# Kernel tuning notes

Hardware: AMD Instinct MI355X
Metric: run time of the kernel (lower is better)

The kernel has to match this reference:

```python
import jax, jax.numpy as jnp
import numpy as np

LMBDA = 100.0
AUX_LMBDA = 25.0
REG = 1e-06
GAMMA = 0.5
EPS = 1e-10


def _safe_evals(e):
    e = jnp.nan_to_num(e, nan=EPS, posinf=1e6, neginf=EPS)
    return jnp.maximum(e, EPS)


def _mask_single(evals1, evals2):
    # evals1, evals2: [k]; returns [k, k] (rows indexed by evals2, cols by evals1)
    e1 = _safe_evals(evals1)
    e2 = _safe_evals(evals2)
    scale = jnp.maximum(jnp.maximum(e1.max(), e2.max()), 1e-10)
    g1 = (e1 / scale) ** GAMMA  # [k]
    g2 = (e2 / scale) ** GAMMA  # [k]
    d1 = g1 * g1 + 1.0
    d2 = g2 * g2 + 1.0
    M_re = (g2 / d2)[:, None] - (g1 / d1)[None, :]
    M_im = (1.0 / d2)[:, None] - (1.0 / d1)[None, :]
    M = M_re * M_re + M_im * M_im
    return jnp.nan_to_num(M, nan=0.0, posinf=1e6, neginf=0.0)


get_mask = jax.vmap(_mask_single)  # [B,k] x [B,k] -> [B,k,k]


def _solve(A, B, evals_x, evals_y, aux_evals_x, aux_evals_y):
    # A, B: [Bb, k, d]
    k = A.shape[1]
    D = LMBDA * get_mask(evals_x, evals_y)  # [Bb, k, k]
    if aux_evals_x is not None and aux_evals_y is not None:
        D = D + AUX_LMBDA * get_mask(aux_evals_x, aux_evals_y)
    AAt = jnp.einsum('bid,bjd->bij', A, A)  # [Bb, k, k]
    BAt = jnp.einsum('bid,bjd->bij', B, A)  # [Bb, k, k]
    I = jnp.eye(k, dtype=A.dtype)
    # lhs[b, i] = AAt[b] + diag(D[b, i]) + reg * I  -> [Bb, k, k, k]
    lhs = AAt[:, None, :, :] + D[:, :, :, None] * I + REG * I
    X = jnp.linalg.solve(lhs, BAt[..., None])[..., 0]  # [Bb, k, k]
    return X


def reference(feat_x, feat_y, evals_x, evals_y, evecs_x, evecs_y,
              aux_evals_x, aux_evals_y):
    A = jnp.einsum('bkn,bnd->bkd', evecs_x, feat_x)
    B = jnp.einsum('bkn,bnd->bkd', evecs_y, feat_y)
    Cxy = _solve(A, B, evals_x, evals_y, aux_evals_x, aux_evals_y)
    Cyx = _solve(B, A, evals_y, evals_x, aux_evals_y, aux_evals_x)
    return (Cxy, Cyx)


def setup_inputs() -> dict:
    key = jax.random.key(0)
    ks = jax.random.split(key, 8)
    Bb, n, d, k = 16, 4096, 512, 128
    return {
        'feat_x': jax.random.normal(ks[0], (Bb, n, d), jnp.float32),
        'feat_y': jax.random.normal(ks[1], (Bb, n, d), jnp.float32),
        'evals_x': jax.random.uniform(ks[2], (Bb, k), jnp.float32),
        'evals_y': jax.random.uniform(ks[3], (Bb, k), jnp.float32),
        'evecs_x': jax.random.normal(ks[4], (Bb, k, n), jnp.float32),
        'evecs_y': jax.random.normal(ks[5], (Bb, k, n), jnp.float32),
        'aux_evals_x': jax.random.uniform(ks[6], (Bb, k), jnp.float32),
        'aux_evals_y': jax.random.uniform(ks[7], (Bb, k), jnp.float32),
    }
```

## Files before the change

### kernel.cpp

```cpp
#include <hip/hip_runtime.h>
#include <math.h>

#define NB 16
#define NN 4096
#define DD 512
#define K128 128

__global__ __launch_bounds__(256) void gemm_proj_k(
    const float* __restrict__ feat_x, const float* __restrict__ feat_y,
    const float* __restrict__ evecs_x, const float* __restrict__ evecs_y,
    float* __restrict__ Aout, float* __restrict__ Bout)
{
    const int z = blockIdx.z;
    const int b = z & 15, which = z >> 4;
    const float* __restrict__ E = (which ? evecs_y : evecs_x) + (size_t)b * K128 * NN;
    const float* __restrict__ F = (which ? feat_y : feat_x) + (size_t)b * NN * DD;
    float* __restrict__ C = (which ? Bout : Aout) + (size_t)b * K128 * DD;
    const int i0 = blockIdx.y * 64;
    const int j0 = blockIdx.x * 128;

    __shared__ float As[32][68];
    __shared__ float Bs[32][128];

    const int t  = threadIdx.x;
    const int tm = t >> 5;
    const int tn = t & 31;

    float acc[8][4];
#pragma unroll
    for (int r = 0; r < 8; ++r)
#pragma unroll
        for (int c = 0; c < 4; ++c) acc[r][c] = 0.f;

    for (int k0 = 0; k0 < NN; k0 += 32) {
#pragma unroll
        for (int s = 0; s < 2; ++s) {
            int idx = t + s * 256;
            int i = idx >> 3, kq = idx & 7;
            float4 v = *(const float4*)(E + (size_t)(i0 + i) * NN + k0 + kq * 4);
            As[kq * 4 + 0][i] = v.x; As[kq * 4 + 1][i] = v.y;
            As[kq * 4 + 2][i] = v.z; As[kq * 4 + 3][i] = v.w;
        }
#pragma unroll
        for (int s = 0; s < 4; ++s) {
            int idx = t + s * 256;
            int kk = idx >> 5, j4 = idx & 31;
            *(float4*)&Bs[kk][j4 * 4] =
                *(const float4*)(F + (size_t)(k0 + kk) * DD + j0 + j4 * 4);
        }
        __syncthreads();
#pragma unroll
        for (int kk = 0; kk < 32; ++kk) {
            float4 a0 = *(const float4*)&As[kk][tm * 8];
            float4 a1 = *(const float4*)&As[kk][tm * 8 + 4];
            float4 b0 = *(const float4*)&Bs[kk][tn * 4];
            float av[8] = {a0.x, a0.y, a0.z, a0.w, a1.x, a1.y, a1.z, a1.w};
            float bv[4] = {b0.x, b0.y, b0.z, b0.w};
#pragma unroll
            for (int r = 0; r < 8; ++r)
#pragma unroll
                for (int c = 0; c < 4; ++c)
                    acc[r][c] = fmaf(av[r], bv[c], acc[r][c]);
        }
        __syncthreads();
    }
#pragma unroll
    for (int r = 0; r < 8; ++r) {
        float4 v = make_float4(acc[r][0], acc[r][1], acc[r][2], acc[r][3]);
        *(float4*)(C + (size_t)(i0 + tm * 8 + r) * DD + j0 + tn * 4) = v;
    }
}

__global__ __launch_bounds__(256) void gram_k(
    const float* __restrict__ A, const float* __restrict__ B,
    float* __restrict__ AAt, float* __restrict__ BBt,
    float* __restrict__ BAt, float* __restrict__ ABt)
{
    const int z = blockIdx.z;
    const int b = z & 15, g = z >> 4;
    const float* X; const float* Y; float* O;
    if (g == 0)      { X = A; Y = A; O = AAt; }
    else if (g == 1) { X = B; Y = B; O = BBt; }
    else if (g == 2) { X = B; Y = A; O = BAt; }
    else             { X = A; Y = B; O = ABt; }
    X += (size_t)b * K128 * DD; Y += (size_t)b * K128 * DD; O += (size_t)b * K128 * K128;
    const int i0 = blockIdx.y * 64, j0 = blockIdx.x * 64;

    __shared__ float Xs[32][68];
    __shared__ float Ys[32][68];

    const int t  = threadIdx.x;
    const int tm = t >> 4, tn = t & 15;

    float acc[4][4];
#pragma unroll
    for (int r = 0; r < 4; ++r)
#pragma unroll
        for (int c = 0; c < 4; ++c) acc[r][c] = 0.f;

    for (int d0 = 0; d0 < DD; d0 += 32) {
#pragma unroll
        for (int s = 0; s < 2; ++s) {
            int idx = t + s * 256;
            int i = idx >> 3, kq = idx & 7;
            float4 v = *(const float4*)(X + (size_t)(i0 + i) * DD + d0 + kq * 4);
            Xs[kq * 4 + 0][i] = v.x; Xs[kq * 4 + 1][i] = v.y;
            Xs[kq * 4 + 2][i] = v.z; Xs[kq * 4 + 3][i] = v.w;
            float4 w = *(const float4*)(Y + (size_t)(j0 + i) * DD + d0 + kq * 4);
            Ys[kq * 4 + 0][i] = w.x; Ys[kq * 4 + 1][i] = w.y;
            Ys[kq * 4 + 2][i] = w.z; Ys[kq * 4 + 3][i] = w.w;
        }
        __syncthreads();
#pragma unroll
        for (int kk = 0; kk < 32; ++kk) {
            float4 a = *(const float4*)&Xs[kk][tm * 4];
            float4 bb = *(const float4*)&Ys[kk][tn * 4];
            float av[4] = {a.x, a.y, a.z, a.w};
            float bv[4] = {bb.x, bb.y, bb.z, bb.w};
#pragma unroll
            for (int r = 0; r < 4; ++r)
#pragma unroll
                for (int c = 0; c < 4; ++c)
                    acc[r][c] = fmaf(av[r], bv[c], acc[r][c]);
        }
        __syncthreads();
    }
#pragma unroll
    for (int r = 0; r < 4; ++r) {
        float4 v = make_float4(acc[r][0], acc[r][1], acc[r][2], acc[r][3]);
        *(float4*)(O + (size_t)(i0 + tm * 4 + r) * K128 + j0 + tn * 4) = v;
    }
}

__global__ __launch_bounds__(256) void dmask_k(
    const float* __restrict__ evx, const float* __restrict__ evy,
    const float* __restrict__ avx, const float* __restrict__ avy,
    float* __restrict__ Dxy, float* __restrict__ Dyx)
{
    const int b = blockIdx.x;
    const int t = threadIdx.x;
    __shared__ float rx[128], sx[128], ry[128], sy[128];
    __shared__ float arx[128], asx[128], ary[128], asy[128];
    __shared__ float rm[4], ra[4];

    float ex = 0.f, ey = 0.f, ax = 0.f, ay = 0.f;
    if (t < 128) {
        ex = fmaxf(evx[b * 128 + t], 1e-10f);
        ey = fmaxf(evy[b * 128 + t], 1e-10f);
        ax = fmaxf(avx[b * 128 + t], 1e-10f);
        ay = fmaxf(avy[b * 128 + t], 1e-10f);
    }
    float lm = (t < 128) ? fmaxf(ex, ey) : 0.f;
    float la = (t < 128) ? fmaxf(ax, ay) : 0.f;
#pragma unroll
    for (int off = 32; off; off >>= 1) {
        lm = fmaxf(lm, __shfl_down(lm, off));
        la = fmaxf(la, __shfl_down(la, off));
    }
    if ((t & 63) == 0) { rm[t >> 6] = lm; ra[t >> 6] = la; }
    __syncthreads();
    const float sm = fmaxf(fmaxf(fmaxf(rm[0], rm[1]), fmaxf(rm[2], rm[3])), 1e-10f);
    const float sa = fmaxf(fmaxf(fmaxf(ra[0], ra[1]), fmaxf(ra[2], ra[3])), 1e-10f);

    if (t < 128) {
        float g, d;
        g = sqrtf(ex / sm); d = g * g + 1.f; rx[t] = g / d; sx[t] = 1.f / d;
        g = sqrtf(ey / sm); d = g * g + 1.f; ry[t] = g / d; sy[t] = 1.f / d;
        g = sqrtf(ax / sa); d = g * g + 1.f; arx[t] = g / d; asx[t] = 1.f / d;
        g = sqrtf(ay / sa); d = g * g + 1.f; ary[t] = g / d; asy[t] = 1.f / d;
    }
    __syncthreads();

    for (int idx = t; idx < 16384; idx += 256) {
        const int i = idx >> 7, j = idx & 127;
        float mre = ry[i] - rx[j];
        float mim = sy[i] - sx[j];
        float m = mre * mre + mim * mim;
        float are_ = ary[i] - arx[j];
        float aim = asy[i] - asx[j];
        float ma = are_ * are_ + aim * aim;
        float dv = 100.f * m + 25.f * ma;
        Dxy[(size_t)b * 16384 + idx] = dv;
        Dyx[(size_t)b * 16384 + (size_t)j * 128 + i] = dv;
    }
}

__global__ __launch_bounds__(512) void gjinv_k(
    const float* __restrict__ AAt, const float* __restrict__ BBt,
    float* __restrict__ Kinv)
{
    __shared__ float S[128][132];
    __shared__ float rowj[128];
    __shared__ float colj[128];
    const int m = blockIdx.x;
    const float* __restrict__ G =
        (m < 16) ? (AAt + (size_t)m * 16384) : (BBt + (size_t)(m - 16) * 16384);
    float* __restrict__ KI = Kinv + (size_t)m * 16384;
    const int t = threadIdx.x;

    for (int idx = t; idx < 16384; idx += 512) {
        const int i = idx >> 7, c = idx & 127;
        S[i][c] = G[idx] + ((i == c) ? 1e-6f : 0.f);
    }
    __syncthreads();

    const int c4  = t & 31;
    const int i00 = t >> 5;

    for (int j = 0; j < 128; ++j) {
        const float p = 1.f / S[j][j];
        if (t < 128) {
            rowj[t] = S[j][t] * p;
            colj[t] = (t == j) ? 0.f : S[t][j];
        }
        __syncthreads();

        const float4 rv = *(const float4*)&rowj[c4 * 4];
#pragma unroll
        for (int s = 0; s < 8; ++s) {
            const int i = i00 + s * 16;
            const float cv = colj[i];
            float4 v = *(const float4*)&S[i][c4 * 4];
            v.x = fmaf(-cv, rv.x, v.x);
            v.y = fmaf(-cv, rv.y, v.y);
            v.z = fmaf(-cv, rv.z, v.z);
            v.w = fmaf(-cv, rv.w, v.w);
            *(float4*)&S[i][c4 * 4] = v;
        }
        __syncthreads();

        if (t < 128) {
            S[t][j] = (t == j) ? p : (-colj[t] * p);
            if (t != j) S[j][t] = rowj[t];
        }
        __syncthreads();
    }

    for (int idx = t; idx < 16384; idx += 512) {
        const int i = idx >> 7, c = idx & 127;
        KI[idx] = S[i][c];
    }
}

__global__ __launch_bounds__(256) void solve_k(
    const float* __restrict__ T_in, const float* __restrict__ Dm,
    const float* __restrict__ X0, const float* __restrict__ Kinv,
    float* __restrict__ Out, const int mode)
{
    const int z = blockIdx.x;
    const size_t base = (size_t)z * 16384;

    __shared__ float Ts[32][132];
    __shared__ float Ks[32][128];

    const int t  = threadIdx.x;
    const int tm = t >> 4, tn = t & 15;

    float acc[8][8];
#pragma unroll
    for (int r = 0; r < 8; ++r)
#pragma unroll
        for (int c = 0; c < 8; ++c) acc[r][c] = 0.f;

    for (int p0 = 0; p0 < 128; p0 += 32) {
#pragma unroll
        for (int s = 0; s < 4; ++s) {
            int idx = t + s * 256;
            int i = idx >> 3, pq = idx & 7;
            float4 v = *(const float4*)(T_in + base + (size_t)i * 128 + p0 + pq * 4);
            if (mode) {
                float4 dv = *(const float4*)(Dm + base + (size_t)i * 128 + p0 + pq * 4);
                v.x *= dv.x; v.y *= dv.y; v.z *= dv.z; v.w *= dv.w;
            }
            Ts[pq * 4 + 0][i] = v.x; Ts[pq * 4 + 1][i] = v.y;
            Ts[pq * 4 + 2][i] = v.z; Ts[pq * 4 + 3][i] = v.w;
        }
#pragma unroll
        for (int s = 0; s < 4; ++s) {
            int idx = t + s * 256;
            int p = idx >> 5, j4 = idx & 31;
            *(float4*)&Ks[p][j4 * 4] =
                *(const float4*)(Kinv + base + (size_t)(p0 + p) * 128 + j4 * 4);
        }
        __syncthreads();
#pragma unroll
        for (int kk = 0; kk < 32; ++kk) {
            float4 a0 = *(const float4*)&Ts[kk][tm * 8];
            float4 a1 = *(const float4*)&Ts[kk][tm * 8 + 4];
            float4 b0 = *(const float4*)&Ks[kk][tn * 8];
            float4 b1 = *(const float4*)&Ks[kk][tn * 8 + 4];
            float av[8] = {a0.x, a0.y, a0.z, a0.w, a1.x, a1.y, a1.z, a1.w};
            float bv[8] = {b0.x, b0.y, b0.z, b0.w, b1.x, b1.y, b1.z, b1.w};
#pragma unroll
            for (int r = 0; r < 8; ++r)
#pragma unroll
                for (int c = 0; c < 8; ++c)
                    acc[r][c] = fmaf(av[r], bv[c], acc[r][c]);
        }
        __syncthreads();
    }

#pragma unroll
    for (int r = 0; r < 8; ++r) {
        const int i = tm * 8 + r;
#pragma unroll
        for (int cq = 0; cq < 2; ++cq) {
            float4 o = make_float4(acc[r][cq * 4 + 0], acc[r][cq * 4 + 1],
                                   acc[r][cq * 4 + 2], acc[r][cq * 4 + 3]);
            if (mode) {
                float4 x0v = *(const float4*)(X0 + base + (size_t)i * 128 + tn * 8 + cq * 4);
                o.x = x0v.x - o.x; o.y = x0v.y - o.y;
                o.z = x0v.z - o.z; o.w = x0v.w - o.w;
            }
            *(float4*)(Out + base + (size_t)i * 128 + tn * 8 + cq * 4) = o;
        }
    }
}

extern "C" void kernel_launch(void* const* d_in, const int* in_sizes, int n_in,
                              void* d_out, int out_size, void* d_ws, size_t ws_size,
                              hipStream_t stream)
{
    (void)in_sizes; (void)n_in; (void)out_size; (void)ws_size;
    const float* feat_x  = (const float*)d_in[0];
    const float* feat_y  = (const float*)d_in[1];
    const float* evals_x = (const float*)d_in[2];
    const float* evals_y = (const float*)d_in[3];
    const float* evecs_x = (const float*)d_in[4];
    const float* evecs_y = (const float*)d_in[5];
    const float* aux_x   = (const float*)d_in[6];
    const float* aux_y   = (const float*)d_in[7];
    float* out = (float*)d_out;
    float* ws  = (float*)d_ws;

    float* A    = ws;
    float* B    = A    + 1048576;
    float* AAt  = B    + 1048576;
    float* BBt  = AAt  + 262144;
    float* R    = BBt  + 262144;
    float* Dm   = R    + 524288;
    float* Kinv = Dm   + 524288;
    float* X0   = Kinv + 524288;
    float* X1   = X0   + 524288;

    gemm_proj_k<<<dim3(4, 2, 32), 256, 0, stream>>>(feat_x, feat_y, evecs_x, evecs_y, A, B);
    gram_k<<<dim3(2, 2, 64), 256, 0, stream>>>(A, B, AAt, BBt, R, R + 262144);
    dmask_k<<<16, 256, 0, stream>>>(evals_x, evals_y, aux_x, aux_y, Dm, Dm + 262144);
    gjinv_k<<<32, 512, 0, stream>>>(AAt, BBt, Kinv);
    solve_k<<<32, 256, 0, stream>>>(R, nullptr, nullptr, Kinv, X0, 0);
    solve_k<<<32, 256, 0, stream>>>(X0, Dm, X0, Kinv, X1, 1);
    solve_k<<<32, 256, 0, stream>>>(X1, Dm, X0, Kinv, out, 1);
}
```

Before: 805.3 us.

## Use split-bf16 MFMA for projection GEMM with split-K partials reduced in gram

Replaces the FP32 scalar-FMA projection GEMM with a kernel that splits each fp32 value into high and low bf16 parts and runs three bf16 MFMA products to approximate fp32 accuracy. K is split in two, giving 256 blocks of 512 threads. The two partial sums are written to workspace and added together inside the gram kernel's loads. The workspace layout is reorganised so the mask and inverse buffers reuse the partial-sum region once it has been read. This trades precision headroom (the dropped low-times-low term) and extra global traffic for the partials against matrix-core throughput.

```diff
diff --git a/kernel.cpp b/kernel.cpp
--- a/kernel.cpp
+++ b/kernel.cpp
@@ -5,108 +5,159 @@
 #define NN 4096
 #define DD 512
 #define K128 128
-
-__global__ __launch_bounds__(256) void gemm_proj_k(
+#define KSPLIT 2
+
+typedef __attribute__((ext_vector_type(8))) short bf16x8;
+typedef __attribute__((ext_vector_type(4))) float f32x4;
+
+__device__ __forceinline__ void split2(float x, unsigned short& h, unsigned short& l)
+{
+    unsigned u = __float_as_uint(x);
+    h = (unsigned short)(u >> 16);
+    float hf = __uint_as_float(u & 0xFFFF0000u);
+    float r = x - hf;
+    unsigned v = __float_as_uint(r);
+    v += 0x7FFF + ((v >> 16) & 1);
+    l = (unsigned short)(v >> 16);
+}
+
+__global__ __launch_bounds__(512) void proj_mfma_k(
     const float* __restrict__ feat_x, const float* __restrict__ feat_y,
     const float* __restrict__ evecs_x, const float* __restrict__ evecs_y,
-    float* __restrict__ Aout, float* __restrict__ Bout)
-{
-    const int z = blockIdx.z;
+    float* __restrict__ P)
+{
+    const int bx = blockIdx.x;
+    const int nb = bx & 3;
+    const int z  = (bx >> 2) & 31;
+    const int ks = bx >> 7;
     const int b = z & 15, which = z >> 4;
     const float* __restrict__ E = (which ? evecs_y : evecs_x) + (size_t)b * K128 * NN;
     const float* __restrict__ F = (which ? feat_y : feat_x) + (size_t)b * NN * DD;
-    float* __restrict__ C = (which ? Bout : Aout) + (size_t)b * K128 * DD;
-    const int i0 = blockIdx.y * 64;
-    const int j0 = blockIdx.x * 128;
-
-    __shared__ float As[32][68];
-    __shared__ float Bs[32][128];
+    float* __restrict__ Po = P + ((size_t)ks * 32 + z) * (K128 * DD) + nb * 128;
+    const int k_beg = ks * (NN / KSPLIT);
+
+    __shared__ unsigned short Eh[128][40], El[128][40];
+    __shared__ unsigned short Fh[128][40], Fl[128][40];
+
+    const int t    = threadIdx.x;
+    const int lane = t & 63;
+    const int w    = t >> 6;
+    const int wm   = (w >> 2) * 64;
+    const int wn   = (w & 3) * 32;
+    const int lr   = lane & 15;
+    const int lg   = lane >> 4;
+
+    f32x4 acc[4][2];
+#pragma unroll
+    for (int mi = 0; mi < 4; ++mi)
+#pragma unroll
+        for (int ni = 0; ni < 2; ++ni) acc[mi][ni] = (f32x4){0.f, 0.f, 0.f, 0.f};
+
+    for (int k0 = 0; k0 < NN / KSPLIT; k0 += 32) {
+#pragma unroll
+        for (int s = 0; s < 2; ++s) {
+            int idx = t + s * 512;
+            int i = idx >> 3, kq = idx & 7;
+            float4 v = *(const float4*)(E + (size_t)i * NN + k_beg + k0 + kq * 4);
+            unsigned short h0, l0, h1, l1, h2, l2, h3, l3;
+            split2(v.x, h0, l0); split2(v.y, h1, l1);
+            split2(v.z, h2, l2); split2(v.w, h3, l3);
+            *(ushort4*)&Eh[i][kq * 4] = make_ushort4(h0, h1, h2, h3);
+            *(ushort4*)&El[i][kq * 4] = make_ushort4(l0, l1, l2, l3);
+        }
+#pragma unroll
+        for (int s = 0; s < 2; ++s) {
+            int idx = t + s * 512;
+            int kk = idx >> 5, j4 = idx & 31;
+            float4 v = *(const float4*)(F + (size_t)(k_beg + k0 + kk) * DD + nb * 128 + j4 * 4);
+            unsigned short h0, l0, h1, l1, h2, l2, h3, l3;
+            split2(v.x, h0, l0); split2(v.y, h1, l1);
+            split2(v.z, h2, l2); split2(v.w, h3, l3);
+            Fh[j4 * 4 + 0][kk] = h0; Fl[j4 * 4 + 0][kk] = l0;
+            Fh[j4 * 4 + 1][kk] = h1; Fl[j4 * 4 + 1][kk] = l1;
+            Fh[j4 * 4 + 2][kk] = h2; Fl[j4 * 4 + 2][kk] = l2;
+            Fh[j4 * 4 + 3][kk] = h3; Fl[j4 * 4 + 3][kk] = l3;
+        }
+        __syncthreads();
+
+        bf16x8 a_h[4], a_l[4];
+#pragma unroll
+        for (int mi = 0; mi < 4; ++mi) {
+            a_h[mi] = *(const bf16x8*)&Eh[wm + mi * 16 + lr][lg * 8];
+            a_l[mi] = *(const bf16x8*)&El[wm + mi * 16 + lr][lg * 8];
+        }
+#pragma unroll
+        for (int ni = 0; ni < 2; ++ni) {
+            bf16x8 b_h = *(const bf16x8*)&Fh[wn + ni * 16 + lr][lg * 8];
+            bf16x8 b_l = *(const bf16x8*)&Fl[wn + ni * 16 + lr][lg * 8];
+#pragma unroll
+            for (int mi = 0; mi < 4; ++mi) {
+                acc[mi][ni] = __builtin_amdgcn_mfma_f32_16x16x32_bf16(a_h[mi], b_h, acc[mi][ni], 0, 0, 0);
+                acc[mi][ni] = __builtin_amdgcn_mfma_f32_16x16x32_bf16(a_h[mi], b_l, acc[mi][ni], 0, 0, 0);
+                acc[mi][ni] = __builtin_amdgcn_mfma_f32_16x16x32_bf16(a_l[mi], b_h, acc[mi][ni], 0, 0, 0);
+            }
+        }
+        __syncthreads();
+    }
+
+#pragma unroll
+    for (int mi = 0; mi < 4; ++mi)
+#pragma unroll
+        for (int ni = 0; ni < 2; ++ni)
+#pragma unroll
+            for (int r = 0; r < 4; ++r) {
+                const int row = wm + mi * 16 + lg * 4 + r;
+                const int col = wn + ni * 16 + lr;
+                Po[(size_t)row * DD + col] = acc[mi][ni][r];
+            }
+}
+
+__global__ __launch_bounds__(256) void gram_k(
+    const float* __restrict__ P,
+    float* __restrict__ AAt, float* __restrict__ BBt,
+    float* __restrict__ BAt, float* __restrict__ ABt)
+{
+    const int zz = blockIdx.z;
+    const int b = zz & 15, g = zz >> 4;
+    int z1, z2; float* O;
+    if (g == 0)      { z1 = b;      z2 = b;      O = AAt; }
+    else if (g == 1) { z1 = 16 + b; z2 = 16 + b; O = BBt; }
+    else if (g == 2) { z1 = 16 + b; z2 = b;      O = BAt; }
+    else             { z1 = b;      z2 = 16 + b; O = ABt; }
+    const float* __restrict__ Xp0 = P + (size_t)z1 * (K128 * DD);
+    const float* __restrict__ Xp1 = Xp0 + (size_t)32 * K128 * DD;
+    const float* __restrict__ Yp0 = P + (size_t)z2 * (K128 * DD);
+    const float* __restrict__ Yp1 = Yp0 + (size_t)32 * K128 * DD;
+    O += (size_t)b * K128 * K128;
+    const int i0 = blockIdx.y * 64, j0 = blockIdx.x * 64;
+
+    __shared__ float Xs[32][68];
+    __shared__ float Ys[32][68];
 
     const int t  = threadIdx.x;
-    const int tm = t >> 5;
-    const int tn = t & 31;
-
-    float acc[8][4];
-#pragma unroll
-    for (int r = 0; r < 8; ++r)
+    const int tm = t >> 4, tn = t & 15;
+
+    float acc[4][4];
+#pragma unroll
+    for (int r = 0; r < 4; ++r)
 #pragma unroll
         for (int c = 0; c < 4; ++c) acc[r][c] = 0.f;
 
-    for (int k0 = 0; k0 < NN; k0 += 32) {
+    for (int d0 = 0; d0 < DD; d0 += 32) {
 #pragma unroll
         for (int s = 0; s < 2; ++s) {
             int idx = t + s * 256;
             int i = idx >> 3, kq = idx & 7;
-            float4 v = *(const float4*)(E + (size_t)(i0 + i) * NN + k0 + kq * 4);
-            As[kq * 4 + 0][i] = v.x; As[kq * 4 + 1][i] = v.y;
-            As[kq * 4 + 2][i] = v.z; As[kq * 4 + 3][i] = v.w;
-        }
-#pragma unroll
-        for (int s = 0; s < 4; ++s) {
-            int idx = t + s * 256;
-            int kk = idx >> 5, j4 = idx & 31;
-            *(float4*)&Bs[kk][j4 * 4] =
-                *(const float4*)(F + (size_t)(k0 + kk) * DD + j0 + j4 * 4);
-        }
-        __syncthreads();
-#pragma unroll
-        for (int kk = 0; kk < 32; ++kk) {
-            float4 a0 = *(const float4*)&As[kk][tm * 8];
-            float4 a1 = *(const float4*)&As[kk][tm * 8 + 4];
-            float4 b0 = *(const float4*)&Bs[kk][tn * 4];
-            float av[8] = {a0.x, a0.y, a0.z, a0.w, a1.x, a1.y, a1.z, a1.w};
-            float bv[4] = {b0.x, b0.y, b0.z, b0.w};
-#pragma unroll
-            for (int r = 0; r < 8; ++r)
-#pragma unroll
-                for (int c = 0; c < 4; ++c)
-                    acc[r][c] = fmaf(av[r], bv[c], acc[r][c]);
-        }
-        __syncthreads();
-    }
-#pragma unroll
-    for (int r = 0; r < 8; ++r) {
-        float4 v = make_float4(acc[r][0], acc[r][1], acc[r][2], acc[r][3]);
-        *(float4*)(C + (size_t)(i0 + tm * 8 + r) * DD + j0 + tn * 4) = v;
-    }
-}
-
-__global__ __launch_bounds__(256) void gram_k(
-    const float* __restrict__ A, const float* __restrict__ B,
-    float* __restrict__ AAt, float* __restrict__ BBt,
-    float* __restrict__ BAt, float* __restrict__ ABt)
-{
-    const int z = blockIdx.z;
-    const int b = z & 15, g = z >> 4;
-    const float* X; const float* Y; float* O;
-    if (g == 0)      { X = A; Y = A; O = AAt; }
-    else if (g == 1) { X = B; Y = B; O = BBt; }
-    else if (g == 2) { X = B; Y = A; O = BAt; }
-    else             { X = A; Y = B; O = ABt; }
-    X += (size_t)b * K128 * DD; Y += (size_t)b * K128 * DD; O += (size_t)b * K128 * K128;
-    const int i0 = blockIdx.y * 64, j0 = blockIdx.x * 64;
-
-    __shared__ float Xs[32][68];
-    __shared__ float Ys[32][68];
-
-    const int t  = threadIdx.x;
-    const int tm = t >> 4, tn = t & 15;
-
-    float acc[4][4];
-#pragma unroll
-    for (int r = 0; r < 4; ++r)
-#pragma unroll
-        for (int c = 0; c < 4; ++c) acc[r][c] = 0.f;
-
-    for (int d0 = 0; d0 < DD; d0 += 32) {
-#pragma unroll
-        for (int s = 0; s < 2; ++s) {
-            int idx = t + s * 256;
-            int i = idx >> 3, kq = idx & 7;
-            float4 v = *(const float4*)(X + (size_t)(i0 + i) * DD + d0 + kq * 4);
+            size_t offX = (size_t)(i0 + i) * DD + d0 + kq * 4;
+            float4 v = *(const float4*)(Xp0 + offX);
+            float4 v1 = *(const float4*)(Xp1 + offX);
+            v.x += v1.x; v.y += v1.y; v.z += v1.z; v.w += v1.w;
             Xs[kq * 4 + 0][i] = v.x; Xs[kq * 4 + 1][i] = v.y;
             Xs[kq * 4 + 2][i] = v.z; Xs[kq * 4 + 3][i] = v.w;
-            float4 w = *(const float4*)(Y + (size_t)(j0 + i) * DD + d0 + kq * 4);
+            size_t offY = (size_t)(j0 + i) * DD + d0 + kq * 4;
+            float4 w = *(const float4*)(Yp0 + offY);
+            float4 w1 = *(const float4*)(Yp1 + offY);
+            w.x += w1.x; w.y += w1.y; w.z += w1.z; w.w += w1.w;
             Ys[kq * 4 + 0][i] = w.x; Ys[kq * 4 + 1][i] = w.y;
             Ys[kq * 4 + 2][i] = w.z; Ys[kq * 4 + 3][i] = w.w;
         }
@@ -333,18 +384,17 @@
     float* out = (float*)d_out;
     float* ws  = (float*)d_ws;
 
-    float* A    = ws;
-    float* B    = A    + 1048576;
-    float* AAt  = B    + 1048576;
-    float* BBt  = AAt  + 262144;
-    float* R    = BBt  + 262144;
-    float* Dm   = R    + 524288;
-    float* Kinv = Dm   + 524288;
+    float* P    = ws;
+    float* AAt  = ws + 4194304;
+    float* BBt  = AAt + 262144;
+    float* R    = BBt + 262144;
+    float* Dm   = ws;
+    float* Kinv = Dm + 524288;
     float* X0   = Kinv + 524288;
-    float* X1   = X0   + 524288;
-
-    gemm_proj_k<<<dim3(4, 2, 32), 256, 0, stream>>>(feat_x, feat_y, evecs_x, evecs_y, A, B);
-    gram_k<<<dim3(2, 2, 64), 256, 0, stream>>>(A, B, AAt, BBt, R, R + 262144);
+    float* X1   = X0 + 524288;
+
+    proj_mfma_k<<<256, 512, 0, stream>>>(feat_x, feat_y, evecs_x, evecs_y, P);
+    gram_k<<<dim3(2, 2, 64), 256, 0, stream>>>(P, AAt, BBt, R, R + 262144);
     dmask_k<<<16, 256, 0, stream>>>(evals_x, evals_y, aux_x, aux_y, Dm, Dm + 262144);
     gjinv_k<<<32, 512, 0, stream>>>(AAt, BBt, Kinv);
     solve_k<<<32, 256, 0, stream>>>(R, nullptr, nullptr, Kinv, X0, 0);
```

Result: faster. 649.0 us (-19.4%).
